# Optimization experiments

Measured on AMD Instinct MI355X. Metric: run time of the kernel, lower is better.

The kernel has to match this reference:

```python
import jax, jax.numpy as jnp
import numpy as np

VAT = 57      # vat_tokens
ACT = 56      # action_num (KV slice start for cross-attn)
H = 16        # num_heads
NG = 3        # n_groups for num_non_act == 768


def setup_inputs() -> dict:
    key = jax.random.key(0)
    ks = jax.random.split(key, 6)
    B, N, C = 64, 825, 1024
    s = 0.02
    return {
        "x": jax.random.normal(ks[0], (B, N, C), dtype=jnp.float32),
        "W_qkv_non": jax.random.normal(ks[1], (C, 3 * C), dtype=jnp.float32) * s,
        "W_q_act": jax.random.normal(ks[2], (C, C), dtype=jnp.float32) * s,
        "W_kv_act": jax.random.normal(ks[3], (C, 2 * C), dtype=jnp.float32) * s,
        "W_proj_non": jax.random.normal(ks[4], (C, C), dtype=jnp.float32) * s,
        "b_proj_non": jnp.zeros((C,), dtype=jnp.float32),
        "W_proj_act": jax.random.normal(ks[5], (C, C), dtype=jnp.float32) * s,
        "b_proj_act": jnp.zeros((C,), dtype=jnp.float32),
    }


def reference(x, W_qkv_non, W_q_act, W_kv_act, W_proj_non, b_proj_non,
              W_proj_act, b_proj_act):
    B, N, C = x.shape
    d = C // H
    scale = d ** -0.5
    nna = N - VAT              # num non-act tokens (768)
    gs = nna // NG             # group size (256)

    # --- grouped windowed self-attention over non-act tokens ---
    non = x[:, VAT:].reshape(B, NG, gs, C)
    qkv = (non @ W_qkv_non).reshape(B, NG, gs, 3, H, d)
    q, k, v = jnp.moveaxis(qkv, 3, 0)           # each [B, NG, gs, H, d]
    q = q.transpose(0, 1, 3, 2, 4)              # [B, NG, H, gs, d]
    k = k.transpose(0, 1, 3, 2, 4)
    v = v.transpose(0, 1, 3, 2, 4)
    attn = jax.nn.softmax(jnp.einsum('bghqd,bghkd->bghqk', q, k) * scale, axis=-1)
    x_non = jnp.einsum('bghqk,bghkd->bghqd', attn, v)
    x_non = x_non.transpose(0, 1, 3, 2, 4).reshape(B, nna, C)

    # --- cross-attention: act queries attend to KV subset [ACT:] of all tokens ---
    q_act = (x[:, :VAT] @ W_q_act).reshape(B, VAT, H, d).transpose(0, 2, 1, 3)
    kv = (x @ W_kv_act).reshape(B, N, 2, H, d)
    k_act = kv[:, ACT:, 0].transpose(0, 2, 1, 3)   # [B, H, N-ACT, d]
    v_act = kv[:, ACT:, 1].transpose(0, 2, 1, 3)
    attn_a = jax.nn.softmax(jnp.einsum('bhqd,bhkd->bhqk', q_act, k_act) * scale, axis=-1)
    x_act = jnp.einsum('bhqk,bhkd->bhqd', attn_a, v_act)
    x_act = x_act.transpose(0, 2, 1, 3).reshape(B, VAT, C)

    # --- output projections + concat [act, non] ---
    x_non = x_non @ W_proj_non + b_proj_non
    x_act = x_act @ W_proj_act + b_proj_act
    return jnp.concatenate([x_act, x_non], axis=1)
```

## Files before the change

kernel.cpp:

```cpp
#include <hip/hip_runtime.h>
#include <stdint.h>


typedef __attribute__((ext_vector_type(8))) unsigned short u16x8;
typedef __attribute__((ext_vector_type(8))) _Float16 f16x8;
typedef __attribute__((ext_vector_type(4))) float f32x4;

__device__ __forceinline__ unsigned short f2h(float f) {
  _Float16 h = (_Float16)f;
  return __builtin_bit_cast(unsigned short, h);
}

__device__ __forceinline__ void mfma16(f32x4& d, u16x8 a, u16x8 b) {
  d = __builtin_amdgcn_mfma_f32_16x16x32_f16(
      __builtin_bit_cast(f16x8, a), __builtin_bit_cast(f16x8, b), d, 0, 0, 0);
}

__device__ __forceinline__ void async16(void* lds_p, const void* g) {
  __builtin_amdgcn_global_load_lds(
      (const __attribute__((address_space(1))) unsigned int*)g,
      (__attribute__((address_space(3))) unsigned int*)lds_p, 16, 0, 0);
}

__device__ __forceinline__ int swz(int row, int bcol) {
  return (row << 7) + (bcol ^ ((row & 7) << 4));
}

static constexpr size_t OFF_XB   = 0;
static constexpr size_t OFF_QKV  = 108134400;
static constexpr size_t OFF_KV   = 410124288;
static constexpr size_t OFF_QACT = 611713024;
static constexpr size_t OFF_ANON = 619184128;
static constexpr size_t OFF_AACT = 719847424;
static constexpr size_t OFF_WQKV = 727318528;
static constexpr size_t OFF_WKV  = 733609984;
static constexpr size_t OFF_WQ   = 737804288;
static constexpr size_t OFF_WPN  = 739901440;
static constexpr size_t OFF_WPA  = 741998592;

__global__ __launch_bounds__(256) void k_cast(const float* __restrict__ in,
                                              unsigned short* __restrict__ outp,
                                              int n8) {
  int stride = gridDim.x * 256;
  for (int i = blockIdx.x * 256 + threadIdx.x; i < n8; i += stride) {
    float4 v0 = ((const float4*)in)[i * 2];
    float4 v1 = ((const float4*)in)[i * 2 + 1];
    uint4 w;
    w.x = (unsigned)f2h(v0.x) | ((unsigned)f2h(v0.y) << 16);
    w.y = (unsigned)f2h(v0.z) | ((unsigned)f2h(v0.w) << 16);
    w.z = (unsigned)f2h(v1.x) | ((unsigned)f2h(v1.y) << 16);
    w.w = (unsigned)f2h(v1.z) | ((unsigned)f2h(v1.w) << 16);
    ((uint4*)outp)[i] = w;
  }
}

__global__ __launch_bounds__(256) void k_tc5(
    const float* __restrict__ Wqkv, const float* __restrict__ Wkv,
    const float* __restrict__ Wq,   const float* __restrict__ Wpn,
    const float* __restrict__ Wpa,
    unsigned short* __restrict__ Tqkv, unsigned short* __restrict__ Tkv,
    unsigned short* __restrict__ Tq,   unsigned short* __restrict__ Tpn,
    unsigned short* __restrict__ Tpa) {
  __shared__ float ts[32][33];
  int bx = blockIdx.x;
  const float* W; unsigned short* Wt; int Nc, nb;
  if (bx < 96)       { W = Wqkv; Wt = Tqkv; Nc = 3072; nb = bx; }
  else if (bx < 160) { W = Wkv;  Wt = Tkv;  Nc = 2048; nb = bx - 96; }
  else if (bx < 192) { W = Wq;   Wt = Tq;   Nc = 1024; nb = bx - 160; }
  else if (bx < 224) { W = Wpn;  Wt = Tpn;  Nc = 1024; nb = bx - 192; }
  else               { W = Wpa;  Wt = Tpa;  Nc = 1024; nb = bx - 224; }
  int n0 = nb * 32, k0 = blockIdx.y * 32;
  int tx = threadIdx.x & 31, ty = threadIdx.x >> 5;
#pragma unroll
  for (int i = 0; i < 4; i++) {
    int k = ty + i * 8;
    ts[k][tx] = W[(size_t)(k0 + k) * Nc + n0 + tx];
  }
  __syncthreads();
#pragma unroll
  for (int i = 0; i < 4; i++) {
    int n = ty + i * 8;
    Wt[(size_t)(n0 + n) * 1024 + k0 + tx] = f2h(ts[tx][n]);
  }
}

template <int EPI>
__global__ __launch_bounds__(512, 2) void k_gemm256(
    const unsigned short* __restrict__ A, const unsigned short* __restrict__ Bt,
    const float* __restrict__ bias, void* __restrict__ outp,
    int M, int NTN, int arpb, int aoff, int ldo, int orpb, int ooff) {
  extern __shared__ char lds[];
  int tid = threadIdx.x, lane = tid & 63, wid = tid >> 6;
  int fr = lane & 15, fg = lane >> 4;

  int nwg = gridDim.x;
  int q8 = nwg >> 3, r8 = nwg & 7;
  int xcd = blockIdx.x & 7, idx = blockIdx.x >> 3;
  int wg = (xcd < r8 ? xcd * (q8 + 1) : r8 * (q8 + 1) + (xcd - r8) * q8) + idx;
  int mt = wg / NTN, nt = wg - mt * NTN;
  int r0 = mt << 8, n0 = nt << 8;

  const unsigned short* pA[2][2];
  const unsigned short* pB[2][2];
#pragma unroll
  for (int j = 0; j < 2; j++) {
    int rc = (wid * 2 + j) * 8 + (lane >> 3);
    int cc = (lane & 7) ^ (rc & 7);
#pragma unroll
    for (int a = 0; a < 2; a++) {
      int row = (rc >> 6) * 128 + a * 64 + (rc & 63);
      int r = r0 + row;
      if (r >= M) r = M - 1;
      size_t gr;
      if (arpb > 0) { int bb = r / arpb; gr = (size_t)bb * 825 + aoff + (r - bb * arpb); }
      else gr = (size_t)r;
      pA[a][j] = A + gr * 1024 + cc * 8;
    }
#pragma unroll
    for (int b = 0; b < 2; b++) {
      int n = ((rc >> 5) & 3) * 64 + b * 32 + (rc & 31);
      pB[b][j] = Bt + (size_t)(n0 + n) * 1024 + cc * 8;
    }
  }

  int wr = wid >> 2, wc = wid & 3;
  int ch0 = fg ^ (fr & 7);
  int aoff0 = (wr * 64 + fr) * 128 + ch0 * 16;
  int boff0 = (wc * 32 + fr) * 128 + ch0 * 16;

  u16x8 afr[8], bf0[4], bf1[4];
  f32x4 acc[8][4] = {};

#define BAR  asm volatile("s_barrier" ::: "memory")
#define VM6  asm volatile("s_waitcnt vmcnt(6)" ::: "memory")
#define VM0  asm volatile("s_waitcnt vmcnt(0)" ::: "memory")

  auto LDA = [&](int d, int a) {
    char* base = lds + d * 65536 + a * 16384;
#pragma unroll
    for (int mm = 0; mm < 4; mm++)
#pragma unroll
      for (int ks = 0; ks < 2; ks++)
        afr[mm * 2 + ks] = *(const u16x8*)(base + mm * 2048 + (aoff0 ^ (ks * 64)));
  };
  auto LDB = [&](int d, int b, u16x8* bf) {
    char* base = lds + d * 65536 + 32768 + b * 16384;
#pragma unroll
    for (int nn = 0; nn < 2; nn++)
#pragma unroll
      for (int ks = 0; ks < 2; ks++)
        bf[nn * 2 + ks] = *(const u16x8*)(base + nn * 2048 + (boff0 ^ (ks * 64)));
  };
  auto STAGE_A = [&](int d, int a, int t) {
#pragma unroll
    for (int j = 0; j < 2; j++)
      async16(lds + d * 65536 + a * 16384 + ((wid * 2 + j) << 10), pA[a][j] + t * 64);
  };
  auto STAGE_B = [&](int d, int b, int t) {
#pragma unroll
    for (int j = 0; j < 2; j++)
      async16(lds + d * 65536 + 32768 + b * 16384 + ((wid * 2 + j) << 10), pB[b][j] + t * 64);
  };
  auto CLUSTER = [&](int a, int b, u16x8* bf) {
    __builtin_amdgcn_s_setprio(1);
#pragma unroll
    for (int mm = 0; mm < 4; mm++)
#pragma unroll
      for (int nn = 0; nn < 2; nn++)
#pragma unroll
        for (int ks = 0; ks < 2; ks++)
          mfma16(acc[a * 4 + mm][b * 2 + nn], afr[mm * 2 + ks], bf[nn * 2 + ks]);
    __builtin_amdgcn_s_setprio(0);
  };

  STAGE_A(0, 0, 0); STAGE_B(0, 0, 0); STAGE_B(0, 1, 0); STAGE_A(0, 1, 0);
  STAGE_A(1, 0, 1); STAGE_B(1, 0, 1); STAGE_B(1, 1, 1);
  VM6; BAR;

#pragma unroll 1
  for (int i = 0; i < 8; i++) {
    bool nl = (i < 7);
    int t1 = 2 * i + 1, t2 = 2 * i + 2, t3 = 2 * i + 3;
    LDA(0, 0); LDB(0, 0, bf0);
    STAGE_A(1, 1, t1);
    CLUSTER(0, 0, bf0); BAR;
    LDB(0, 1, bf1);
    if (nl) STAGE_A(0, 0, t2);
    CLUSTER(0, 1, bf1);
    LDA(0, 1);
    if (nl) STAGE_B(0, 0, t2);
    CLUSTER(1, 0, bf0); BAR;
    if (nl) STAGE_B(0, 1, t2);
    CLUSTER(1, 1, bf1);
    if (nl) { VM6; } else { VM0; }
    BAR;
    LDA(1, 0); LDB(1, 0, bf0);
    if (nl) STAGE_A(0, 1, t2);
    CLUSTER(0, 0, bf0); BAR;
    LDB(1, 1, bf1);
    if (nl) STAGE_A(1, 0, t3);
    CLUSTER(0, 1, bf1);
    LDA(1, 1);
    if (nl) STAGE_B(1, 0, t3);
    CLUSTER(1, 0, bf0); BAR;
    if (nl) STAGE_B(1, 1, t3);
    CLUSTER(1, 1, bf1);
    if (nl) { VM6; } else { VM0; }
    BAR;
  }
#undef BAR
#undef VM6
#undef VM0

  int coln[4];
#pragma unroll
  for (int n = 0; n < 4; n++)
    coln[n] = n0 + wc * 64 + (n >> 1) * 32 + (n & 1) * 16 + fr;
  if (EPI == 0) {
    unsigned short* o = (unsigned short*)outp;
#pragma unroll
    for (int m = 0; m < 8; m++)
#pragma unroll
      for (int reg = 0; reg < 4; reg++) {
        int r = r0 + wr * 128 + (m >> 2) * 64 + (m & 3) * 16 + (lane >> 4) * 4 + reg;
        if (r < M) {
          size_t base = (size_t)r * ldo;
#pragma unroll
          for (int n = 0; n < 4; n++) o[base + coln[n]] = f2h(acc[m][n][reg]);
        }
      }
  } else {
    float* o = (float*)outp;
#pragma unroll
    for (int m = 0; m < 8; m++)
#pragma unroll
      for (int reg = 0; reg < 4; reg++) {
        int r = r0 + wr * 128 + (m >> 2) * 64 + (m & 3) * 16 + (lane >> 4) * 4 + reg;
        if (r < M) {
          int bb = r / orpb;
          size_t orow = (size_t)bb * 825 + ooff + (r - bb * orpb);
          size_t base = orow * 1024;
#pragma unroll
          for (int n = 0; n < 4; n++)
            o[base + coln[n]] = acc[m][n][reg] + bias[coln[n]];
        }
      }
  }
}

template <int EPI>
__global__ __launch_bounds__(256, 2) void k_gemm(
    const unsigned short* __restrict__ A, const unsigned short* __restrict__ Bt,
    const float* __restrict__ bias, void* __restrict__ outp,
    int M, int Nn, int arpb, int aoff, int ldo, int orpb, int ooff) {
  __shared__ __align__(16) unsigned short As[128 * 32];
  __shared__ __align__(16) unsigned short Bs[128 * 32];
  int tid = threadIdx.x, lane = tid & 63, wid = tid >> 6;
  int NT = Nn >> 7;
  int mt = blockIdx.x / NT, nt = blockIdx.x - mt * NT;
  int r0 = mt << 7, n0 = nt << 7;

  const unsigned short* aptr[2];
  const unsigned short* bptr[2];
#pragma unroll
  for (int i = 0; i < 2; i++) {
    int c = tid + (i << 8);
    int r = r0 + (c >> 2);
    if (r >= M) r = M - 1;
    size_t gr;
    if (arpb > 0) { int bb = r / arpb; gr = (size_t)bb * 825 + aoff + (r - bb * arpb); }
    else gr = (size_t)r;
    aptr[i] = A + gr * 1024 + (c & 3) * 8;
    bptr[i] = Bt + (size_t)(n0 + (c >> 2)) * 1024 + (c & 3) * 8;
  }
  char* AsB = (char*)As;
  char* BsB = (char*)Bs;
  int wr = wid >> 1, wc = wid & 1;
  int fr = lane & 15, fcol = (lane >> 4) * 16;
  f32x4 acc[4][4] = {};

  for (int kk = 0; kk < 1024; kk += 32) {
    async16(AsB + (wid << 10), aptr[0] + kk);
    async16(AsB + 4096 + (wid << 10), aptr[1] + kk);
    async16(BsB + (wid << 10), bptr[0] + kk);
    async16(BsB + 4096 + (wid << 10), bptr[1] + kk);
    __syncthreads();
    u16x8 af[4], bfv[4];
#pragma unroll
    for (int m = 0; m < 4; m++)
      af[m] = *(const u16x8*)(AsB + (wr * 64 + m * 16 + fr) * 64 + fcol);
#pragma unroll
    for (int n = 0; n < 4; n++)
      bfv[n] = *(const u16x8*)(BsB + (wc * 64 + n * 16 + fr) * 64 + fcol);
#pragma unroll
    for (int m = 0; m < 4; m++)
#pragma unroll
      for (int n = 0; n < 4; n++) mfma16(acc[m][n], af[m], bfv[n]);
    __syncthreads();
  }

  int cb = wc * 64 + fr;
  int rb = wr * 64 + (lane >> 4) * 4;
  if (EPI == 0) {
    unsigned short* o = (unsigned short*)outp;
#pragma unroll
    for (int m = 0; m < 4; m++)
#pragma unroll
      for (int reg = 0; reg < 4; reg++) {
        int r = r0 + rb + m * 16 + reg;
        if (r < M) {
          size_t base = (size_t)r * ldo + n0 + cb;
#pragma unroll
          for (int n = 0; n < 4; n++) o[base + n * 16] = f2h(acc[m][n][reg]);
        }
      }
  } else {
    float* o = (float*)outp;
#pragma unroll
    for (int m = 0; m < 4; m++)
#pragma unroll
      for (int reg = 0; reg < 4; reg++) {
        int r = r0 + rb + m * 16 + reg;
        if (r < M) {
          int bb = r / orpb;
          size_t orow = (size_t)bb * 825 + ooff + (r - bb * orpb);
          size_t base = orow * 1024 + n0 + cb;
#pragma unroll
          for (int n = 0; n < 4; n++)
            o[base + n * 16] = acc[m][n][reg] + bias[n0 + cb + n * 16];
        }
      }
  }
}

__global__ __launch_bounds__(256, 2) void k_attn_non(
    const unsigned short* __restrict__ qkv, unsigned short* __restrict__ aout) {
  int bid = blockIdx.x;
  int h = bid & 15, t = bid >> 4;
  int g = t % 3, b = t / 3;
  int tid = threadIdx.x, lane = tid & 63, wid = tid >> 6;
  int fr = lane & 15, fg = lane >> 4;
  size_t rowbase = (size_t)(b * 768 + g * 256);
  const unsigned short* Qb = qkv + rowbase * 3072 + h * 64;
  const unsigned short* Kb = Qb + 1024;
  const unsigned short* Vb = Qb + 2048;

  __shared__ __align__(16) unsigned short Vts[64 * 64];
  __shared__ __align__(16) unsigned short Ps[4][64 * 64];
  char* VtB = (char*)Vts;
  char* Pw = (char*)Ps[wid];

  int qr = wid * 64;
  u16x8 qf[4][2];
#pragma unroll
  for (int mq = 0; mq < 4; mq++)
#pragma unroll
    for (int ks = 0; ks < 2; ks++)
      qf[mq][ks] = *(const u16x8*)(Qb + (size_t)(qr + mq * 16 + fr) * 3072 + ks * 32 + fg * 8);

  f32x4 o[4][4] = {};
  float mrun[4], lrun[4];
#pragma unroll
  for (int mq = 0; mq < 4; mq++) { mrun[mq] = -1e30f; lrun[mq] = 0.f; }
  const float c1 = 0.125f * 1.44269504089f;

  int vpr = tid >> 3, vcc = tid & 7;
  u16x8 v0 = *(const u16x8*)(Vb + (size_t)(2 * vpr) * 3072 + vcc * 8);
  u16x8 v1 = *(const u16x8*)(Vb + (size_t)(2 * vpr + 1) * 3072 + vcc * 8);

  for (int c = 0; c < 4; c++) {
    __syncthreads();
    u16x8 kf[2][4];
#pragma unroll
    for (int kt = 0; kt < 4; kt++)
#pragma unroll
      for (int ks = 0; ks < 2; ks++)
        kf[ks][kt] = *(const u16x8*)(Kb + (size_t)(c * 64 + kt * 16 + fr) * 3072 + ks * 32 + fg * 8);
#pragma unroll
    for (int j = 0; j < 8; j++) {
      unsigned pk = (unsigned)v0[j] | ((unsigned)v1[j] << 16);
      *(unsigned*)(VtB + swz(vcc * 8 + j, 4 * vpr)) = pk;
    }
    if (c < 3) {
      v0 = *(const u16x8*)(Vb + (size_t)((c + 1) * 64 + 2 * vpr) * 3072 + vcc * 8);
      v1 = *(const u16x8*)(Vb + (size_t)((c + 1) * 64 + 2 * vpr + 1) * 3072 + vcc * 8);
    }

    f32x4 s[4][4] = {};
#pragma unroll
    for (int ks = 0; ks < 2; ks++)
#pragma unroll
      for (int kt = 0; kt < 4; kt++)
#pragma unroll
        for (int mq = 0; mq < 4; mq++) mfma16(s[kt][mq], kf[ks][kt], qf[mq][ks]);
#pragma unroll
    for (int kt = 0; kt < 4; kt++)
#pragma unroll
      for (int mq = 0; mq < 4; mq++) s[kt][mq] *= c1;

#pragma unroll
    for (int mq = 0; mq < 4; mq++) {
      float v = -1e30f;
#pragma unroll
      for (int kt = 0; kt < 4; kt++)
#pragma unroll
        for (int reg = 0; reg < 4; reg++) v = fmaxf(v, s[kt][mq][reg]);
      v = fmaxf(v, __shfl_xor(v, 16));
      v = fmaxf(v, __shfl_xor(v, 32));
      float mn = fmaxf(mrun[mq], v);
      float alpha = exp2f(mrun[mq] - mn);
      mrun[mq] = mn;
      int q = mq * 16 + fr;
      float rs = 0.f;
#pragma unroll
      for (int kt = 0; kt < 4; kt++) {
        f32x4 p;
#pragma unroll
        for (int reg = 0; reg < 4; reg++) p[reg] = exp2f(s[kt][mq][reg] - mn);
        rs += p[0] + p[1] + p[2] + p[3];
        uint2 w;
        w.x = (unsigned)f2h(p[0]) | ((unsigned)f2h(p[1]) << 16);
        w.y = (unsigned)f2h(p[2]) | ((unsigned)f2h(p[3]) << 16);
        *(uint2*)(Pw + swz(q, kt * 32 + fg * 8)) = w;
      }
      rs += __shfl_xor(rs, 16);
      rs += __shfl_xor(rs, 32);
      lrun[mq] = lrun[mq] * alpha + rs;
#pragma unroll
      for (int dt = 0; dt < 4; dt++) o[dt][mq] *= alpha;
    }
    __syncthreads();
#pragma unroll
    for (int ks = 0; ks < 2; ks++) {
      u16x8 vf[4], pf[4];
#pragma unroll
      for (int dt = 0; dt < 4; dt++)
        vf[dt] = *(const u16x8*)(VtB + swz(dt * 16 + fr, ks * 64 + fg * 16));
#pragma unroll
      for (int mq = 0; mq < 4; mq++)
        pf[mq] = *(const u16x8*)(Pw + swz(mq * 16 + fr, ks * 64 + fg * 16));
#pragma unroll
      for (int dt = 0; dt < 4; dt++)
#pragma unroll
        for (int mq = 0; mq < 4; mq++) mfma16(o[dt][mq], vf[dt], pf[mq]);
    }
  }

#pragma unroll
  for (int mq = 0; mq < 4; mq++) {
    float rl = 1.0f / lrun[mq];
    size_t row = rowbase + qr + mq * 16 + fr;
#pragma unroll
    for (int dt = 0; dt < 4; dt++) {
      uint2 w;
      w.x = (unsigned)f2h(o[dt][mq][0] * rl) | ((unsigned)f2h(o[dt][mq][1] * rl) << 16);
      w.y = (unsigned)f2h(o[dt][mq][2] * rl) | ((unsigned)f2h(o[dt][mq][3] * rl) << 16);
      *(uint2*)(aout + row * 1024 + h * 64 + dt * 16 + fg * 4) = w;
    }
  }
}

__global__ __launch_bounds__(256, 2) void k_attn_act(
    const unsigned short* __restrict__ qa, const unsigned short* __restrict__ kv,
    unsigned short* __restrict__ aout) {
  int bid = blockIdx.x;
  int h = bid & 15, b = bid >> 4;
  int tid = threadIdx.x, lane = tid & 63, wid = tid >> 6;
  int fr = lane & 15, fg = lane >> 4;
  const unsigned short* Qb = qa + (size_t)b * 57 * 1024 + h * 64;
  const unsigned short* Kb = kv + (size_t)b * 769 * 2048 + h * 64;
  const unsigned short* Vb = Kb + 1024;

  __shared__ __align__(16) unsigned short Vts[4][64 * 64];
  __shared__ __align__(16) unsigned short Ps[4][64 * 64];
  __shared__ float Ml[4][64], Ll[4][64];
  char* Vw = (char*)Vts[wid];
  char* Pw = (char*)Ps[wid];

  u16x8 qf[4][2];
#pragma unroll
  for (int mq = 0; mq < 4; mq++) {
    int q = mq * 16 + fr;
    if (q > 56) q = 56;
#pragma unroll
    for (int ks = 0; ks < 2; ks++)
      qf[mq][ks] = *(const u16x8*)(Qb + (size_t)q * 1024 + ks * 32 + fg * 8);
  }
  f32x4 o[4][4] = {};
  float mrun[4], lrun[4];
#pragma unroll
  for (int mq = 0; mq < 4; mq++) { mrun[mq] = -1e30f; lrun[mq] = 0.f; }
  const float c1 = 0.125f * 1.44269504089f;

  for (int c = wid; c < 13; c += 4) {
    int kc0 = c * 64;
    u16x8 kf[2][4];
#pragma unroll
    for (int kt = 0; kt < 4; kt++) {
      int krow = kc0 + kt * 16 + fr;
      if (krow > 768) krow = 768;
#pragma unroll
      for (int ks = 0; ks < 2; ks++)
        kf[ks][kt] = *(const u16x8*)(Kb + (size_t)krow * 2048 + ks * 32 + fg * 8);
    }
#pragma unroll
    for (int i = 0; i < 4; i++) {
      int idx = lane + i * 64;
      int pr = idx >> 3, cv = idx & 7;
      int kr0 = kc0 + 2 * pr, kr1 = kc0 + 2 * pr + 1;
      if (kr0 > 768) kr0 = 768;
      if (kr1 > 768) kr1 = 768;
      u16x8 v0 = *(const u16x8*)(Vb + (size_t)kr0 * 2048 + cv * 8);
      u16x8 v1 = *(const u16x8*)(Vb + (size_t)kr1 * 2048 + cv * 8);
#pragma unroll
      for (int j = 0; j < 8; j++) {
        unsigned pk = (unsigned)v0[j] | ((unsigned)v1[j] << 16);
        *(unsigned*)(Vw + swz(cv * 8 + j, 4 * pr)) = pk;
      }
    }

    f32x4 s[4][4] = {};
#pragma unroll
    for (int ks = 0; ks < 2; ks++)
#pragma unroll
      for (int kt = 0; kt < 4; kt++)
#pragma unroll
        for (int mq = 0; mq < 4; mq++) mfma16(s[kt][mq], kf[ks][kt], qf[mq][ks]);
#pragma unroll
    for (int kt = 0; kt < 4; kt++)
#pragma unroll
      for (int mq = 0; mq < 4; mq++) s[kt][mq] *= c1;
    if (kc0 + 64 > 769) {
#pragma unroll
      for (int kt = 0; kt < 4; kt++)
#pragma unroll
        for (int reg = 0; reg < 4; reg++)
          if (kc0 + kt * 16 + fg * 4 + reg >= 769)
#pragma unroll
            for (int mq = 0; mq < 4; mq++) s[kt][mq][reg] = -1e30f;
    }

#pragma unroll
    for (int mq = 0; mq < 4; mq++) {
      float v = -1e30f;
#pragma unroll
      for (int kt = 0; kt < 4; kt++)
#pragma unroll
        for (int reg = 0; reg < 4; reg++) v = fmaxf(v, s[kt][mq][reg]);
      v = fmaxf(v, __shfl_xor(v, 16));
      v = fmaxf(v, __shfl_xor(v, 32));
      float mn = fmaxf(mrun[mq], v);
      float alpha = exp2f(mrun[mq] - mn);
      mrun[mq] = mn;
      int q = mq * 16 + fr;
      float rs = 0.f;
#pragma unroll
      for (int kt = 0; kt < 4; kt++) {
        f32x4 p;
#pragma unroll
        for (int reg = 0; reg < 4; reg++) p[reg] = exp2f(s[kt][mq][reg] - mn);
        rs += p[0] + p[1] + p[2] + p[3];
        uint2 w;
        w.x = (unsigned)f2h(p[0]) | ((unsigned)f2h(p[1]) << 16);
        w.y = (unsigned)f2h(p[2]) | ((unsigned)f2h(p[3]) << 16);
        *(uint2*)(Pw + swz(q, kt * 32 + fg * 8)) = w;
      }
      rs += __shfl_xor(rs, 16);
      rs += __shfl_xor(rs, 32);
      lrun[mq] = lrun[mq] * alpha + rs;
#pragma unroll
      for (int dt = 0; dt < 4; dt++) o[dt][mq] *= alpha;
    }
#pragma unroll
    for (int ks = 0; ks < 2; ks++) {
      u16x8 vf[4], pf[4];
#pragma unroll
      for (int dt = 0; dt < 4; dt++)
        vf[dt] = *(const u16x8*)(Vw + swz(dt * 16 + fr, ks * 64 + fg * 16));
#pragma unroll
      for (int mq = 0; mq < 4; mq++)
        pf[mq] = *(const u16x8*)(Pw + swz(mq * 16 + fr, ks * 64 + fg * 16));
#pragma unroll
      for (int dt = 0; dt < 4; dt++)
#pragma unroll
        for (int mq = 0; mq < 4; mq++) mfma16(o[dt][mq], vf[dt], pf[mq]);
    }
  }

  __syncthreads();
  if (fg == 0) {
#pragma unroll
    for (int mq = 0; mq < 4; mq++) {
      Ml[wid][mq * 16 + fr] = mrun[mq];
      Ll[wid][mq * 16 + fr] = lrun[mq];
    }
  }
  __syncthreads();
  float* Oac = (float*)&Vts[0][0];
  for (int i = tid; i < 4096; i += 256) Oac[i] = 0.f;
  __syncthreads();
  for (int w = 0; w < 4; w++) {
    if (wid == w) {
#pragma unroll
      for (int mq = 0; mq < 4; mq++) {
        int q = mq * 16 + fr;
        float Mq = fmaxf(fmaxf(Ml[0][q], Ml[1][q]), fmaxf(Ml[2][q], Ml[3][q]));
        float f = exp2f(mrun[mq] - Mq);
#pragma unroll
        for (int dt = 0; dt < 4; dt++) {
          int d = dt * 16 + fg * 4;
#pragma unroll
          for (int reg = 0; reg < 4; reg++)
            Oac[(d + reg) * 64 + q] += o[dt][mq][reg] * f;
        }
      }
    }
    __syncthreads();
  }
  for (int i = tid; i < 4096; i += 256) {
    int d = i >> 6, q = i & 63;
    if (q < 57) {
      float Mq = fmaxf(fmaxf(Ml[0][q], Ml[1][q]), fmaxf(Ml[2][q], Ml[3][q]));
      float Lq = Ll[0][q] * exp2f(Ml[0][q] - Mq) + Ll[1][q] * exp2f(Ml[1][q] - Mq) +
                 Ll[2][q] * exp2f(Ml[2][q] - Mq) + Ll[3][q] * exp2f(Ml[3][q] - Mq);
      aout[(size_t)(b * 57 + q) * 1024 + h * 64 + d] = f2h(Oac[i] / Lq);
    }
  }
}

extern "C" void kernel_launch(void* const* d_in, const int* in_sizes, int n_in,
                              void* d_out, int out_size, void* d_ws, size_t ws_size,
                              hipStream_t stream) {
  const float* x    = (const float*)d_in[0];
  const float* Wqkv = (const float*)d_in[1];
  const float* Wq   = (const float*)d_in[2];
  const float* Wkv  = (const float*)d_in[3];
  const float* Wpn  = (const float*)d_in[4];
  const float* bpn  = (const float*)d_in[5];
  const float* Wpa  = (const float*)d_in[6];
  const float* bpa  = (const float*)d_in[7];
  float* out = (float*)d_out;
  char* ws = (char*)d_ws;

  unsigned short* xb   = (unsigned short*)(ws + OFF_XB);
  unsigned short* qkv  = (unsigned short*)(ws + OFF_QKV);
  unsigned short* kvb  = (unsigned short*)(ws + OFF_KV);
  unsigned short* qact = (unsigned short*)(ws + OFF_QACT);
  unsigned short* anon = (unsigned short*)(ws + OFF_ANON);
  unsigned short* aact = (unsigned short*)(ws + OFF_AACT);
  unsigned short* WtQKV = (unsigned short*)(ws + OFF_WQKV);
  unsigned short* WtKV  = (unsigned short*)(ws + OFF_WKV);
  unsigned short* WtQ   = (unsigned short*)(ws + OFF_WQ);
  unsigned short* WtPN  = (unsigned short*)(ws + OFF_WPN);
  unsigned short* WtPA  = (unsigned short*)(ws + OFF_WPA);

  hipFuncSetAttribute((const void*)k_gemm256<0>,
                      hipFuncAttributeMaxDynamicSharedMemorySize, 131072);
  hipFuncSetAttribute((const void*)k_gemm256<1>,
                      hipFuncAttributeMaxDynamicSharedMemorySize, 131072);

  k_cast<<<2048, 256, 0, stream>>>(x, xb, 6758400);
  k_tc5<<<dim3(256, 32), 256, 0, stream>>>(Wqkv, Wkv, Wq, Wpn, Wpa,
                                           WtQKV, WtKV, WtQ, WtPN, WtPA);

  k_gemm256<0><<<192 * 12, 512, 131072, stream>>>(xb, WtQKV, nullptr, qkv,
                                                  49152, 12, 768, 57, 3072, 0, 0);
  k_gemm256<0><<<193 * 8, 512, 131072, stream>>>(xb, WtKV, nullptr, kvb,
                                                 49216, 8, 769, 56, 2048, 0, 0);
  k_gemm<0><<<29 * 8, 256, 0, stream>>>(xb, WtQ, nullptr, qact,
                                        3648, 1024, 57, 0, 1024, 0, 0);

  k_attn_non<<<64 * 3 * 16, 256, 0, stream>>>(qkv, anon);
  k_attn_act<<<64 * 16, 256, 0, stream>>>(qact, kvb, aact);

  k_gemm256<1><<<192 * 4, 512, 131072, stream>>>(anon, WtPN, bpn, out,
                                                 49152, 4, 0, 0, 1024, 768, 57);
  k_gemm<1><<<29 * 8, 256, 0, stream>>>(aact, WtPA, bpa, out,
                                        3648, 1024, 0, 0, 1024, 57, 0);
}
```

Before: 1.004 ms.

## Fuse input GEMMs into one launch, prefetch K tiles, use raw exp2

```diff
diff --git a/kernel.cpp b/kernel.cpp
--- a/kernel.cpp
+++ b/kernel.cpp
@@ -9,6 +9,10 @@
 __device__ __forceinline__ unsigned short f2h(float f) {
   _Float16 h = (_Float16)f;
   return __builtin_bit_cast(unsigned short, h);
+}
+
+__device__ __forceinline__ float exp2r(float x) {
+  return __builtin_amdgcn_exp2f(x);
 }
 
 __device__ __forceinline__ void mfma16(f32x4& d, u16x8 a, u16x8 b) {
@@ -24,6 +28,12 @@
 
 __device__ __forceinline__ int swz(int row, int bcol) {
   return (row << 7) + (bcol ^ ((row & 7) << 4));
+}
+
+__device__ __forceinline__ int xcd_swz(int bid, int nwg) {
+  int q8 = nwg >> 3, r8 = nwg & 7;
+  int xcd = bid & 7, idx = bid >> 3;
+  return (xcd < r8 ? xcd * (q8 + 1) : r8 * (q8 + 1) + (xcd - r8) * q8) + idx;
 }
 
 static constexpr size_t OFF_XB   = 0;
@@ -85,20 +95,17 @@
 }
 
 template <int EPI>
-__global__ __launch_bounds__(512, 2) void k_gemm256(
+__device__ __forceinline__ void gemm256_body(
     const unsigned short* __restrict__ A, const unsigned short* __restrict__ Bt,
     const float* __restrict__ bias, void* __restrict__ outp,
-    int M, int NTN, int arpb, int aoff, int ldo, int orpb, int ooff) {
-  extern __shared__ char lds[];
+    int M, int NTN, int arpb, int aoff, int ldo, int orpb, int ooff,
+    int wg, char* lds) {
   int tid = threadIdx.x, lane = tid & 63, wid = tid >> 6;
   int fr = lane & 15, fg = lane >> 4;
 
-  int nwg = gridDim.x;
-  int q8 = nwg >> 3, r8 = nwg & 7;
-  int xcd = blockIdx.x & 7, idx = blockIdx.x >> 3;
-  int wg = (xcd < r8 ? xcd * (q8 + 1) : r8 * (q8 + 1) + (xcd - r8) * q8) + idx;
   int mt = wg / NTN, nt = wg - mt * NTN;
   int r0 = mt << 8, n0 = nt << 8;
+  if (r0 > M - 256) r0 = M - 256;
 
   const unsigned short* pA[2][2];
   const unsigned short* pB[2][2];
@@ -248,6 +255,37 @@
   }
 }
 
+__global__ __launch_bounds__(512, 2) void k_gemm_in(
+    const unsigned short* __restrict__ xb,
+    const unsigned short* __restrict__ WtQKV,
+    const unsigned short* __restrict__ WtKV,
+    const unsigned short* __restrict__ WtQ,
+    unsigned short* __restrict__ qkv, unsigned short* __restrict__ kvb,
+    unsigned short* __restrict__ qact) {
+  extern __shared__ char lds[];
+  int bid = blockIdx.x;
+  if (bid < 2304) {
+    gemm256_body<0>(xb, WtQKV, nullptr, qkv, 49152, 12, 768, 57, 3072, 0, 0,
+                    xcd_swz(bid, 2304), lds);
+  } else if (bid < 3848) {
+    gemm256_body<0>(xb, WtKV, nullptr, kvb, 49216, 8, 769, 56, 2048, 0, 0,
+                    xcd_swz(bid - 2304, 1544), lds);
+  } else {
+    gemm256_body<0>(xb, WtQ, nullptr, qact, 3648, 4, 57, 0, 1024, 0, 0,
+                    xcd_swz(bid - 3848, 60), lds);
+  }
+}
+
+template <int EPI>
+__global__ __launch_bounds__(512, 2) void k_gemm256(
+    const unsigned short* __restrict__ A, const unsigned short* __restrict__ Bt,
+    const float* __restrict__ bias, void* __restrict__ outp,
+    int M, int NTN, int arpb, int aoff, int ldo, int orpb, int ooff) {
+  extern __shared__ char lds[];
+  gemm256_body<EPI>(A, Bt, bias, outp, M, NTN, arpb, aoff, ldo, orpb, ooff,
+                    xcd_swz(blockIdx.x, gridDim.x), lds);
+}
+
 template <int EPI>
 __global__ __launch_bounds__(256, 2) void k_gemm(
     const unsigned short* __restrict__ A, const unsigned short* __restrict__ Bt,
@@ -367,15 +405,15 @@
   int vpr = tid >> 3, vcc = tid & 7;
   u16x8 v0 = *(const u16x8*)(Vb + (size_t)(2 * vpr) * 3072 + vcc * 8);
   u16x8 v1 = *(const u16x8*)(Vb + (size_t)(2 * vpr + 1) * 3072 + vcc * 8);
+  u16x8 kf[2][4];
+#pragma unroll
+  for (int kt = 0; kt < 4; kt++)
+#pragma unroll
+    for (int ks = 0; ks < 2; ks++)
+      kf[ks][kt] = *(const u16x8*)(Kb + (size_t)(kt * 16 + fr) * 3072 + ks * 32 + fg * 8);
 
   for (int c = 0; c < 4; c++) {
     __syncthreads();
-    u16x8 kf[2][4];
-#pragma unroll
-    for (int kt = 0; kt < 4; kt++)
-#pragma unroll
-      for (int ks = 0; ks < 2; ks++)
-        kf[ks][kt] = *(const u16x8*)(Kb + (size_t)(c * 64 + kt * 16 + fr) * 3072 + ks * 32 + fg * 8);
 #pragma unroll
     for (int j = 0; j < 8; j++) {
       unsigned pk = (unsigned)v0[j] | ((unsigned)v1[j] << 16);
@@ -393,6 +431,13 @@
       for (int kt = 0; kt < 4; kt++)
 #pragma unroll
         for (int mq = 0; mq < 4; mq++) mfma16(s[kt][mq], kf[ks][kt], qf[mq][ks]);
+    if (c < 3) {
+#pragma unroll
+      for (int kt = 0; kt < 4; kt++)
+#pragma unroll
+        for (int ks = 0; ks < 2; ks++)
+          kf[ks][kt] = *(const u16x8*)(Kb + (size_t)((c + 1) * 64 + kt * 16 + fr) * 3072 + ks * 32 + fg * 8);
+    }
 #pragma unroll
     for (int kt = 0; kt < 4; kt++)
 #pragma unroll
@@ -408,7 +453,7 @@
       v = fmaxf(v, __shfl_xor(v, 16));
       v = fmaxf(v, __shfl_xor(v, 32));
       float mn = fmaxf(mrun[mq], v);
-      float alpha = exp2f(mrun[mq] - mn);
+      float alpha = exp2r(mrun[mq] - mn);
       mrun[mq] = mn;
       int q = mq * 16 + fr;
       float rs = 0.f;
@@ -416,7 +461,7 @@
       for (int kt = 0; kt < 4; kt++) {
         f32x4 p;
 #pragma unroll
-        for (int reg = 0; reg < 4; reg++) p[reg] = exp2f(s[kt][mq][reg] - mn);
+        for (int reg = 0; reg < 4; reg++) p[reg] = exp2r(s[kt][mq][reg] - mn);
         rs += p[0] + p[1] + p[2] + p[3];
         uint2 w;
         w.x = (unsigned)f2h(p[0]) | ((unsigned)f2h(p[1]) << 16);
@@ -492,9 +537,9 @@
   for (int mq = 0; mq < 4; mq++) { mrun[mq] = -1e30f; lrun[mq] = 0.f; }
   const float c1 = 0.125f * 1.44269504089f;
 
-  for (int c = wid; c < 13; c += 4) {
-    int kc0 = c * 64;
-    u16x8 kf[2][4];
+  u16x8 kf[2][4];
+  {
+    int kc0 = wid * 64;
 #pragma unroll
     for (int kt = 0; kt < 4; kt++) {
       int krow = kc0 + kt * 16 + fr;
@@ -503,6 +548,10 @@
       for (int ks = 0; ks < 2; ks++)
         kf[ks][kt] = *(const u16x8*)(Kb + (size_t)krow * 2048 + ks * 32 + fg * 8);
     }
+  }
+
+  for (int c = wid; c < 13; c += 4) {
+    int kc0 = c * 64;
 #pragma unroll
     for (int i = 0; i < 4; i++) {
       int idx = lane + i * 64;
@@ -526,6 +575,17 @@
       for (int kt = 0; kt < 4; kt++)
 #pragma unroll
         for (int mq = 0; mq < 4; mq++) mfma16(s[kt][mq], kf[ks][kt], qf[mq][ks]);
+    if (c + 4 < 13) {
+      int kn = (c + 4) * 64;
+#pragma unroll
+      for (int kt = 0; kt < 4; kt++) {
+        int krow = kn + kt * 16 + fr;
+        if (krow > 768) krow = 768;
+#pragma unroll
+        for (int ks = 0; ks < 2; ks++)
+          kf[ks][kt] = *(const u16x8*)(Kb + (size_t)krow * 2048 + ks * 32 + fg * 8);
+      }
+    }
 #pragma unroll
     for (int kt = 0; kt < 4; kt++)
 #pragma unroll
@@ -550,7 +610,7 @@
       v = fmaxf(v, __shfl_xor(v, 16));
       v = fmaxf(v, __shfl_xor(v, 32));
       float mn = fmaxf(mrun[mq], v);
-      float alpha = exp2f(mrun[mq] - mn);
+      float alpha = exp2r(mrun[mq] - mn);
       mrun[mq] = mn;
       int q = mq * 16 + fr;
       float rs = 0.f;
@@ -558,7 +618,7 @@
       for (int kt = 0; kt < 4; kt++) {
         f32x4 p;
 #pragma unroll
-        for (int reg = 0; reg < 4; reg++) p[reg] = exp2f(s[kt][mq][reg] - mn);
+        for (int reg = 0; reg < 4; reg++) p[reg] = exp2r(s[kt][mq][reg] - mn);
         rs += p[0] + p[1] + p[2] + p[3];
         uint2 w;
         w.x = (unsigned)f2h(p[0]) | ((unsigned)f2h(p[1]) << 16);
@@ -605,7 +665,7 @@
       for (int mq = 0; mq < 4; mq++) {
         int q = mq * 16 + fr;
         float Mq = fmaxf(fmaxf(Ml[0][q], Ml[1][q]), fmaxf(Ml[2][q], Ml[3][q]));
-        float f = exp2f(mrun[mq] - Mq);
+        float f = exp2r(mrun[mq] - Mq);
 #pragma unroll
         for (int dt = 0; dt < 4; dt++) {
           int d = dt * 16 + fg * 4;
@@ -621,8 +681,8 @@
     int d = i >> 6, q = i & 63;
     if (q < 57) {
       float Mq = fmaxf(fmaxf(Ml[0][q], Ml[1][q]), fmaxf(Ml[2][q], Ml[3][q]));
-      float Lq = Ll[0][q] * exp2f(Ml[0][q] - Mq) + Ll[1][q] * exp2f(Ml[1][q] - Mq) +
-                 Ll[2][q] * exp2f(Ml[2][q] - Mq) + Ll[3][q] * exp2f(Ml[3][q] - Mq);
+      float Lq = Ll[0][q] * exp2r(Ml[0][q] - Mq) + Ll[1][q] * exp2r(Ml[1][q] - Mq) +
+                 Ll[2][q] * exp2r(Ml[2][q] - Mq) + Ll[3][q] * exp2r(Ml[3][q] - Mq);
       aout[(size_t)(b * 57 + q) * 1024 + h * 64 + d] = f2h(Oac[i] / Lq);
     }
   }
@@ -654,7 +714,7 @@
   unsigned short* WtPN  = (unsigned short*)(ws + OFF_WPN);
   unsigned short* WtPA  = (unsigned short*)(ws + OFF_WPA);
 
-  hipFuncSetAttribute((const void*)k_gemm256<0>,
+  hipFuncSetAttribute((const void*)k_gemm_in,
                       hipFuncAttributeMaxDynamicSharedMemorySize, 131072);
   hipFuncSetAttribute((const void*)k_gemm256<1>,
                       hipFuncAttributeMaxDynamicSharedMemorySize, 131072);
@@ -663,12 +723,8 @@
   k_tc5<<<dim3(256, 32), 256, 0, stream>>>(Wqkv, Wkv, Wq, Wpn, Wpa,
                                            WtQKV, WtKV, WtQ, WtPN, WtPA);
 
-  k_gemm256<0><<<192 * 12, 512, 131072, stream>>>(xb, WtQKV, nullptr, qkv,
-                                                  49152, 12, 768, 57, 3072, 0, 0);
-  k_gemm256<0><<<193 * 8, 512, 131072, stream>>>(xb, WtKV, nullptr, kvb,
-                                                 49216, 8, 769, 56, 2048, 0, 0);
-  k_gemm<0><<<29 * 8, 256, 0, stream>>>(xb, WtQ, nullptr, qact,
-                                        3648, 1024, 57, 0, 1024, 0, 0);
+  k_gemm_in<<<3908, 512, 131072, stream>>>(xb, WtQKV, WtKV, WtQ,
+                                           qkv, kvb, qact);
 
   k_attn_non<<<64 * 3 * 16, 256, 0, stream>>>(qkv, anon);
   k_attn_act<<<64 * 16, 256, 0, stream>>>(qact, kvb, aact);
```

Result: faster. 980.6 us (-2.3%).
